# Kernel optimization log

Hardware: AMD Instinct MI355X
Metric: run time of the kernel (lower is better)

The kernel has to match this reference:

```python
import jax, jax.numpy as jnp
import numpy as np

K = 16          # num clusters
DZ = 64         # dim_zt == dim_zi (required by decoder matmul)
DT = 1024       # treatment feature dim (dim_t)
NT = 2048       # number of treatments == dim_x (columns of input_ins)
NI = 4096       # number of instances
MU_P_WT = 5.0
COS_EPS = 1e-6


def setup_inputs() -> dict:
    key = jax.random.key(0)
    ks = jax.random.split(key, 12)
    s = 0.02
    return {
        "input_ins": jax.random.uniform(ks[0], (NI, NT), dtype=jnp.float32),
        "input_treat": jax.random.normal(ks[1], (NT, DT), dtype=jnp.float32),
        # nn.Linear params (torch layout: W [out, in], y = x @ W.T + b)
        "W_mu_zt": jax.random.normal(ks[2], (DZ, DT)) * s,
        "b_mu_zt": jnp.zeros((DZ,), jnp.float32),
        "W_lv_zt": jax.random.normal(ks[3], (DZ, DT)) * s,
        "b_lv_zt": jnp.zeros((DZ,), jnp.float32),
        "W_arec": jax.random.normal(ks[4], (DT, DZ)) * s,
        "b_arec": jnp.zeros((DT,), jnp.float32),
        "W_mu_zi": jax.random.normal(ks[5], (DZ, NT)) * s,
        "b_mu_zi": jnp.zeros((DZ,), jnp.float32),
        "W_lv_zi": jax.random.normal(ks[6], (DZ, NT)) * s,
        "b_lv_zi": jnp.zeros((DZ,), jnp.float32),
        "mu_p_zt": jax.random.normal(ks[7], (K, DZ), dtype=jnp.float32),
        "logvar_p_zt": jnp.ones((K, DZ), jnp.float32),
        "W_y1": jax.random.normal(ks[8], (K * DZ, DZ)) * s,
        "b_y1": jnp.zeros((K * DZ,), jnp.float32),
        "W_y2": jax.random.normal(ks[9], (1, K * DZ)) * s,
        "b_y2": jnp.zeros((1,), jnp.float32),
    }


def reference(input_ins, input_treat, W_mu_zt, b_mu_zt, W_lv_zt, b_lv_zt,
              W_arec, b_arec, W_mu_zi, b_mu_zi, W_lv_zi, b_lv_zi,
              mu_p_zt, logvar_p_zt, W_y1, b_y1, W_y2, b_y2):
    # encode_t (eval mode: zt_sample = mu_zt)
    mu_zt = input_treat @ W_mu_zt.T + b_mu_zt           # [NT, DZ]
    logvar_zt = input_treat @ W_lv_zt.T + b_lv_zt       # [NT, DZ]
    zt = mu_zt

    # compute_qc (cosine similarity vs scaled cluster centers, *10)
    centers = MU_P_WT * mu_p_zt                          # [K, DZ]
    num = zt @ centers.T                                 # [NT, K]
    denom = jnp.maximum(
        jnp.linalg.norm(zt, axis=1, keepdims=True) * jnp.linalg.norm(centers, axis=1)[None, :],
        COS_EPS)
    qc_raw = 10.0 * num / denom                          # [NT, K]
    cates = jax.nn.softmax(qc_raw, axis=1)               # forward softmaxes qc once
    c_sample = jax.nn.softmax(cates, axis=1)             # encode_i (eval) softmaxes again

    # encode_i, vectorized over K clusters: (input_ins * cates_k) @ W.T + b
    # fused einsum avoids materializing the [K, NI, NT] masked inputs
    mu_zi = jnp.einsum('nt,tk,dt->knd', input_ins, c_sample, W_mu_zi) + b_mu_zi       # [K, NI, DZ]
    logvar_zi = jnp.einsum('nt,tk,dt->knd', input_ins, c_sample, W_lv_zi) + b_lv_zi   # [K, NI, DZ]
    zi = mu_zi  # eval-mode reparameterize

    # a_reconstby_zt
    a_reconst = jax.nn.sigmoid(zt @ W_arec.T + b_arec)   # [NT, DT]

    # decoder: sum_k sigmoid(zi_k @ zt.T) * cates_k
    logits = jnp.einsum('knd,td->knt', zi, zt)           # [K, NI, NT]
    a_pred = jnp.einsum('knt,tk->nt', jax.nn.sigmoid(logits), c_sample)  # [NI, NT]

    # predictY
    zi_all = jnp.transpose(zi, (1, 0, 2)).reshape(zi.shape[1], K * DZ)   # cat over k, dim=1
    a_zt = input_ins @ zt                                # [NI, DZ]
    rep_w1 = a_zt @ W_y1.T + b_y1                        # [NI, K*DZ]
    pred_y2 = zi_all @ W_y2.T + b_y2                     # [NI, 1]
    # diag(rep_w1 @ zi_all.T) == rowwise dot product (no NIxNI matmul)
    mu_y = jnp.sum(rep_w1 * zi_all, axis=1, keepdims=True) + pred_y2     # [NI, 1]
    logvar_y = jnp.ones_like(mu_y)

    return (mu_zt, logvar_zt, mu_p_zt, logvar_p_zt, cates, mu_zi, logvar_zi,
            zi, a_pred, mu_y, logvar_y, a_reconst)
```

## Files before the change

### kernel.cpp

```cpp
#include <hip/hip_runtime.h>

typedef unsigned short ushort_t;
typedef unsigned int   uint32;
typedef __attribute__((ext_vector_type(8))) short short8;
typedef __attribute__((ext_vector_type(4))) float f32x4;

#define DEV __device__ __forceinline__

#define KC 16
#define DZ 64
#define DT 1024
#define NT 2048
#define NI 4096
#define KD 1024

#define O_MU_ZT   0
#define O_LV_ZT   131072
#define O_MU_P    262144
#define O_LV_P    263168
#define O_CATES   264192
#define O_MU_ZI   296960
#define O_LV_ZI   4491264
#define O_ZI      8685568
#define O_APRED   12879872
#define O_MU_Y    21268480
#define O_LV_Y    21272576
#define O_AREC    21276672

#define WSF_ZT   0
#define WSF_C    131072
#define WSF_CT   163840
#define WSF_AZT  196608
#define WSF_END  458752
#define WSU_ZTB  0
#define WSU_BC   131072
#define WSU_ZIB  4325376
#define WSU_INSB 8519680
#define WSU_ZHT  16908288
#define WSU_ZLT  17039360

DEV ushort_t f2b(float f){
  uint32 u = __float_as_uint(f);
  u += 0x7fffu + ((u >> 16) & 1u);
  return (ushort_t)(u >> 16);
}
DEV uint32 pk(float lo, float hi){
  return (__float_as_uint(hi) & 0xffff0000u) | (__float_as_uint(lo) >> 16);
}
DEV float wred64(float v){
#pragma unroll
  for (int m = 32; m; m >>= 1) v += __shfl_xor(v, m, 64);
  return v;
}
DEV float fastrcp(float x){ return __builtin_amdgcn_rcpf(x); }
DEV void gl2lds16(ushort_t* l, const ushort_t* g){
  __builtin_amdgcn_global_load_lds(
      (const __attribute__((address_space(1))) unsigned int*)g,
      (__attribute__((address_space(3))) unsigned int*)l, 16, 0, 0);
}

__global__ __launch_bounds__(256) void k_encode_t(
    const float* __restrict__ treat, const float* __restrict__ Wmu,
    const float* __restrict__ bmu, const float* __restrict__ Wlv,
    const float* __restrict__ blv, float* __restrict__ out,
    float* __restrict__ ws_zt)
{
  __shared__ float rowsh[8 * DT];
  const int n0 = blockIdx.x * 8, tid = threadIdx.x;
  const float4* src = (const float4*)(treat + (size_t)n0 * DT);
#pragma unroll
  for (int i = 0; i < 8; ++i)
    ((float4*)rowsh)[tid + i * 256] = src[tid + i * 256];
  __syncthreads();
  const int j = tid & 127, half = tid >> 7;
  const bool isMu = j < 64;
  const int jj = j & 63;
  const float* W = (isMu ? Wmu : Wlv) + (size_t)jj * DT;
  const float bias = isMu ? bmu[jj] : blv[jj];
  float a0 = bias, a1 = bias, a2 = bias, a3 = bias;
  const float4* w4 = (const float4*)W;
  const float4* r0 = (const float4*)&rowsh[(half*4 + 0) * DT];
  const float4* r1 = (const float4*)&rowsh[(half*4 + 1) * DT];
  const float4* r2 = (const float4*)&rowsh[(half*4 + 2) * DT];
  const float4* r3 = (const float4*)&rowsh[(half*4 + 3) * DT];
#pragma unroll 4
  for (int i = 0; i < DT / 4; ++i){
    float4 wv = w4[i];
    float4 v0 = r0[i], v1 = r1[i], v2 = r2[i], v3 = r3[i];
    a0 += wv.x*v0.x + wv.y*v0.y + wv.z*v0.z + wv.w*v0.w;
    a1 += wv.x*v1.x + wv.y*v1.y + wv.z*v1.z + wv.w*v1.w;
    a2 += wv.x*v2.x + wv.y*v2.y + wv.z*v2.z + wv.w*v2.w;
    a3 += wv.x*v3.x + wv.y*v3.y + wv.z*v3.z + wv.w*v3.w;
  }
  float acc[4] = {a0, a1, a2, a3};
#pragma unroll
  for (int r = 0; r < 4; ++r){
    const int row = n0 + half*4 + r;
    if (isMu){ out[O_MU_ZT + row*DZ + jj] = acc[r]; ws_zt[row*DZ + jj] = acc[r]; }
    else     { out[O_LV_ZT + row*DZ + jj] = acc[r]; }
  }
}

__global__ __launch_bounds__(256) void k_qc(
    const float* __restrict__ mu_p, const float* __restrict__ ws_zt,
    float* __restrict__ out, float* __restrict__ ws_c, float* __restrict__ ws_cT)
{
  const int tid = threadIdx.x, lane = tid & 63;
  const int row = blockIdx.x * 4 + (tid >> 6);
  const float z = ws_zt[row * DZ + lane];
  const float nz = sqrtf(wred64(z * z));
  float myqc = 0.f;
#pragma unroll
  for (int k = 0; k < KC; ++k){
    float cv  = 5.f * mu_p[k * DZ + lane];
    float dot = wred64(z * cv);
    float nc2 = wred64(cv * cv);
    float qc  = 10.f * dot / fmaxf(nz * sqrtf(nc2), 1e-6f);
    if (lane == k) myqc = qc;
  }
  float mx = myqc;
#pragma unroll
  for (int m = 8; m; m >>= 1) mx = fmaxf(mx, __shfl_xor(mx, m, 16));
  float e = __expf(myqc - mx);
  float s = e;
#pragma unroll
  for (int m = 8; m; m >>= 1) s += __shfl_xor(s, m, 16);
  float cates = e / s;
  float mx2 = cates;
#pragma unroll
  for (int m = 8; m; m >>= 1) mx2 = fmaxf(mx2, __shfl_xor(mx2, m, 16));
  float e2 = __expf(cates - mx2);
  float s2 = e2;
#pragma unroll
  for (int m = 8; m; m >>= 1) s2 += __shfl_xor(s2, m, 16);
  float c2 = e2 / s2;
  if (lane < KC){
    out[O_CATES + row * KC + lane] = cates;
    ws_c[row * KC + lane] = c2;
    ws_cT[lane * NT + row] = c2;
  }
}

__global__ __launch_bounds__(256) void k_prep(
    const float* __restrict__ Wmu, const float* __restrict__ Wlv,
    const float* __restrict__ cT, const float* __restrict__ zt,
    const float* __restrict__ ins,
    ushort_t* __restrict__ Bc, ushort_t* __restrict__ ztb,
    ushort_t* __restrict__ insb,
    ushort_t* __restrict__ zhT, ushort_t* __restrict__ zlT,
    const float* __restrict__ mu_p, const float* __restrict__ lv_p,
    float* __restrict__ out)
{
  const int bx = blockIdx.x, tid = threadIdx.x;
  if (bx < 2048){
    const int j = bx;
    const bool isMu = j < KD;
    const int kk = (j & (KD-1)) >> 6, d = j & 63;
    const float* W = (isMu ? Wmu : Wlv) + (size_t)d * NT;
    const float* c = cT + (size_t)kk * NT;
    const int t = tid * 8;
    float4 w0 = *(const float4*)(W + t), w1 = *(const float4*)(W + t + 4);
    float4 c0 = *(const float4*)(c + t), c1 = *(const float4*)(c + t + 4);
    ushort_t v[8];
    v[0]=f2b(w0.x*c0.x); v[1]=f2b(w0.y*c0.y); v[2]=f2b(w0.z*c0.z); v[3]=f2b(w0.w*c0.w);
    v[4]=f2b(w1.x*c1.x); v[5]=f2b(w1.y*c1.y); v[6]=f2b(w1.z*c1.z); v[7]=f2b(w1.w*c1.w);
    *(uint4*)(Bc + (size_t)j * NT + t) = *(uint4*)v;
  } else if (bx < 2080){
    const int g = (bx - 2048) * 256 + tid;
    const int base = g * 16;
    const float4* src = (const float4*)(zt + base);
    float4 z0 = src[0], z1 = src[1], z2 = src[2], z3 = src[3];
    ushort_t v[16];
    v[0]=f2b(z0.x); v[1]=f2b(z0.y); v[2]=f2b(z0.z); v[3]=f2b(z0.w);
    v[4]=f2b(z1.x); v[5]=f2b(z1.y); v[6]=f2b(z1.z); v[7]=f2b(z1.w);
    v[8]=f2b(z2.x); v[9]=f2b(z2.y); v[10]=f2b(z2.z); v[11]=f2b(z2.w);
    v[12]=f2b(z3.x); v[13]=f2b(z3.y); v[14]=f2b(z3.z); v[15]=f2b(z3.w);
    *(uint4*)(ztb + base) = *(uint4*)&v[0];
    *(uint4*)(ztb + base + 8) = *(uint4*)&v[8];
  } else if (bx < 2084){
    const int i = (bx - 2080) * 256 + tid;
    out[O_MU_P + i] = mu_p[i];
    out[O_LV_P + i] = lv_p[i];
  } else if (bx < 4132){
    const int g = (bx - 2084) * 256 + tid;
    const int base = g * 16;
    const float4* src = (const float4*)(ins + base);
    float4 z0 = src[0], z1 = src[1], z2 = src[2], z3 = src[3];
    ushort_t v[16];
    v[0]=f2b(z0.x); v[1]=f2b(z0.y); v[2]=f2b(z0.z); v[3]=f2b(z0.w);
    v[4]=f2b(z1.x); v[5]=f2b(z1.y); v[6]=f2b(z1.z); v[7]=f2b(z1.w);
    v[8]=f2b(z2.x); v[9]=f2b(z2.y); v[10]=f2b(z2.z); v[11]=f2b(z2.w);
    v[12]=f2b(z3.x); v[13]=f2b(z3.y); v[14]=f2b(z3.z); v[15]=f2b(z3.w);
    *(uint4*)(insb + base) = *(uint4*)&v[0];
    *(uint4*)(insb + base + 8) = *(uint4*)&v[8];
  } else {
    __shared__ float zsh[64 * 65];
    const int t0 = (bx - 4132) * 64;
#pragma unroll
    for (int jj = 0; jj < 16; ++jj){
      const int idx = jj * 256 + tid;
      const int t = idx >> 6, d = idx & 63;
      zsh[t * 65 + d] = zt[(size_t)(t0 + t) * DZ + d];
    }
    __syncthreads();
    const int d = tid >> 2, tq = tid & 3;
    ushort_t vh[16], vl[16];
#pragma unroll
    for (int i = 0; i < 16; ++i){
      const float f = zsh[(tq * 16 + i) * 65 + d];
      const uint32 u = __float_as_uint(f);
      vh[i] = (ushort_t)(u >> 16);
      const float hf = __uint_as_float(u & 0xffff0000u);
      vl[i] = (ushort_t)(__float_as_uint(f - hf) >> 16);
    }
    *(uint4*)(zhT + (size_t)d * NT + t0 + tq * 16)     = *(uint4*)&vh[0];
    *(uint4*)(zhT + (size_t)d * NT + t0 + tq * 16 + 8) = *(uint4*)&vh[8];
    *(uint4*)(zlT + (size_t)d * NT + t0 + tq * 16)     = *(uint4*)&vl[0];
    *(uint4*)(zlT + (size_t)d * NT + t0 + tq * 16 + 8) = *(uint4*)&vl[8];
  }
}

__global__ __launch_bounds__(256) void k_encode_i(
    const ushort_t* __restrict__ insb, const ushort_t* __restrict__ Bc,
    const float* __restrict__ bmu, const float* __restrict__ blv,
    float* __restrict__ out, ushort_t* __restrict__ zib)
{
  __shared__ ushort_t As[2*128*64];
  __shared__ ushort_t Bs[2*128*64];
  const int tid = threadIdx.x;
  const int orig = blockIdx.y * 16 + blockIdx.x;
  const int swz  = (orig & 7) * 64 + (orig >> 3);
  const int j0 = (swz & 15) * 128, n0 = (swz >> 4) * 128;
  const int w = tid >> 6, lane = tid & 63;
  const int wm = w & 1, wn = w >> 1;
  const int l16 = lane & 15, quad = lane >> 4;

  const int srow = tid >> 3, schunk = (tid & 7) ^ (srow & 7);
  const ushort_t* aSrc = insb + (size_t)(n0 + srow) * NT + schunk * 8;
  const ushort_t* bSrc = Bc  + (size_t)(j0 + srow) * NT + schunk * 8;

  f32x4 acc[4][4] = {};

#pragma unroll
  for (int i = 0; i < 4; ++i){
    gl2lds16(&As[tid*8] + i * 2048, aSrc + (size_t)i * 32 * NT);
    gl2lds16(&Bs[tid*8] + i * 2048, bSrc + (size_t)i * 32 * NT);
  }
  __syncthreads();

  int cur = 0;
  for (int kt = 0; kt < NT/64; ++kt){
    if (kt < NT/64 - 1){
      const ushort_t* ak = aSrc + (kt+1) * 64;
      const ushort_t* bk = bSrc + (kt+1) * 64;
      ushort_t* ad = &As[(cur^1)*8192 + tid*8];
      ushort_t* bd = &Bs[(cur^1)*8192 + tid*8];
#pragma unroll
      for (int i = 0; i < 4; ++i){
        gl2lds16(ad + i * 2048, ak + (size_t)i * 32 * NT);
        gl2lds16(bd + i * 2048, bk + (size_t)i * 32 * NT);
      }
    }
    const ushort_t* Ab = &As[cur*8192];
    const ushort_t* Bb = &Bs[cur*8192];
#pragma unroll
    for (int ks = 0; ks < 2; ++ks){
      const int rsw = ((ks*4 + quad) ^ (l16 & 7)) * 8;
      short8 af[4], bf[4];
#pragma unroll
      for (int mf = 0; mf < 4; ++mf)
        af[mf] = *(const short8*)&Ab[(wm*64 + mf*16 + l16)*64 + rsw];
#pragma unroll
      for (int nf = 0; nf < 4; ++nf)
        bf[nf] = *(const short8*)&Bb[(wn*64 + nf*16 + l16)*64 + rsw];
      __builtin_amdgcn_s_setprio(1);
#pragma unroll
      for (int mf = 0; mf < 4; ++mf)
#pragma unroll
        for (int nf = 0; nf < 4; ++nf)
          acc[mf][nf] = __builtin_amdgcn_mfma_f32_16x16x32_bf16(af[mf], bf[nf], acc[mf][nf], 0, 0, 0);
      __builtin_amdgcn_s_setprio(0);
    }
    __syncthreads();
    cur ^= 1;
  }

  const int colW = j0 + wn * 64;
  const bool isMu = colW < KD;
  const int kk = (colW & (KD - 1)) >> 6;
  const float* bias = isMu ? bmu : blv;
  const size_t zbase = (size_t)kk * (NI * DZ);
#pragma unroll
  for (int mf = 0; mf < 4; ++mf){
    const int r = n0 + wm*64 + mf*16 + quad*4;
#pragma unroll
    for (int nf = 0; nf < 4; ++nf){
      const int d = nf*16 + l16;
      const float bv = bias[d];
#pragma unroll
      for (int reg = 0; reg < 4; ++reg){
        float v = acc[mf][nf][reg] + bv;
        size_t idx = zbase + (size_t)(r + reg)*DZ + d;
        if (isMu){
          out[O_MU_ZI + idx] = v;
          out[O_ZI + idx] = v;
          zib[idx] = f2b(v);
        } else {
          out[O_LV_ZI + idx] = v;
        }
      }
    }
  }
}

__global__ __launch_bounds__(256) void k_decoder(
    const ushort_t* __restrict__ ztb, const ushort_t* __restrict__ zib,
    const float* __restrict__ ws_c, float* __restrict__ out)
{
  __shared__ ushort_t Zt[64*64];
  __shared__ ushort_t Zi[128*64];
  __shared__ float ct[64*17];
  const int tid = threadIdx.x;
  const int t0 = blockIdx.x * 64, n0 = blockIdx.y * 128;
  const int w = tid >> 6, lane = tid & 63;
  const int wm = w & 1, wn = w >> 1;
  const int l16 = lane & 15, quad = lane >> 4;
  const int zr = tid >> 2, zq = tid & 3;
  const int ir = tid >> 1, ih = tid & 1;
  {
    const uint4* src = (const uint4*)(ztb + (size_t)(t0 + zr)*DZ + zq*16);
    uint4 z0 = src[0], z1 = src[1];
    ushort_t* dst = &Zt[zr*64];
    *(uint4*)&dst[((zq*2 + 0) ^ (zr & 7)) * 8] = z0;
    *(uint4*)&dst[((zq*2 + 1) ^ (zr & 7)) * 8] = z1;
  }
  for (int i = tid; i < 64*16; i += 256){
    int t = i >> 4, k = i & 15;
    ct[t*17 + k] = ws_c[(size_t)(t0 + t)*KC + k];
  }
  const ushort_t* iG = zib + (size_t)(n0 + ir)*DZ + ih*32;
  ushort_t* isw = &Zi[ir*64];
  const int sw0 = ((ih*4 + 0) ^ (ir & 7)) * 8;
  const int sw1 = ((ih*4 + 1) ^ (ir & 7)) * 8;
  const int sw2 = ((ih*4 + 2) ^ (ir & 7)) * 8;
  const int sw3 = ((ih*4 + 3) ^ (ir & 7)) * 8;
  uint4 Zr0, Zr1, Zr2, Zr3;
  {
    const uint4* zp = (const uint4*)iG;
    Zr0 = zp[0]; Zr1 = zp[1]; Zr2 = zp[2]; Zr3 = zp[3];
  }
  f32x4 accum[4][2] = {};
  for (int k = 0; k < KC; ++k){
    __syncthreads();
    *(uint4*)&isw[sw0] = Zr0; *(uint4*)&isw[sw1] = Zr1;
    *(uint4*)&isw[sw2] = Zr2; *(uint4*)&isw[sw3] = Zr3;
    __syncthreads();
    if (k < KC - 1){
      const uint4* zp = (const uint4*)(iG + (size_t)(k+1)*(NI*DZ));
      Zr0 = zp[0]; Zr1 = zp[1]; Zr2 = zp[2]; Zr3 = zp[3];
    }
    f32x4 s[4][2] = {};
#pragma unroll
    for (int ks = 0; ks < 2; ++ks){
      const int rsw = ((ks*4 + quad) ^ (l16 & 7)) * 8;
      short8 af[4], bf[2];
#pragma unroll
      for (int mf = 0; mf < 4; ++mf)
        af[mf] = *(const short8*)&Zi[(wm*64 + mf*16 + l16)*64 + rsw];
#pragma unroll
      for (int nf = 0; nf < 2; ++nf)
        bf[nf] = *(const short8*)&Zt[(wn*32 + nf*16 + l16)*64 + rsw];
#pragma unroll
      for (int mf = 0; mf < 4; ++mf)
#pragma unroll
        for (int nf = 0; nf < 2; ++nf)
          s[mf][nf] = __builtin_amdgcn_mfma_f32_16x16x32_bf16(af[mf], bf[nf], s[mf][nf], 0, 0, 0);
    }
#pragma unroll
    for (int nf = 0; nf < 2; ++nf){
      const float cv = ct[(wn*32 + nf*16 + l16)*17 + k];
#pragma unroll
      for (int mf = 0; mf < 4; ++mf)
#pragma unroll
        for (int reg = 0; reg < 4; ++reg)
          accum[mf][nf][reg] += cv * fastrcp(1.f + __expf(-s[mf][nf][reg]));
    }
  }
#pragma unroll
  for (int mf = 0; mf < 4; ++mf){
    const int r = n0 + wm*64 + mf*16 + quad*4;
#pragma unroll
    for (int nf = 0; nf < 2; ++nf){
      const int col = t0 + wn*32 + nf*16 + l16;
#pragma unroll
      for (int reg = 0; reg < 4; ++reg)
        out[O_APRED + (size_t)(r + reg)*NT + col] = accum[mf][nf][reg];
    }
  }
}

__global__ __launch_bounds__(256) void k_arec(
    const float* __restrict__ ws_zt, const float* __restrict__ W,
    const float* __restrict__ bias, float* __restrict__ out)
{
  __shared__ float zsh[8 * DZ];
  const int n0 = blockIdx.x * 8, tid = threadIdx.x;
  if (tid < 128)
    ((float4*)zsh)[tid] = ((const float4*)(ws_zt + (size_t)n0 * DZ))[tid];
  __syncthreads();
#pragma unroll
  for (int jo = 0; jo < 4; ++jo){
    const int j = jo*256 + tid;
    const float4* w4 = (const float4*)(W + (size_t)j * DZ);
    const float b = bias[j];
    float acc[8];
#pragma unroll
    for (int r = 0; r < 8; ++r) acc[r] = b;
#pragma unroll
    for (int i = 0; i < 16; ++i){
      float4 wv = w4[i];
#pragma unroll
      for (int r = 0; r < 8; ++r){
        const float* z = &zsh[r*DZ + i*4];
        acc[r] += wv.x*z[0] + wv.y*z[1] + wv.z*z[2] + wv.w*z[3];
      }
    }
#pragma unroll
    for (int r = 0; r < 8; ++r)
      out[O_AREC + (size_t)(n0 + r)*DT + j] = fastrcp(1.f + __expf(-acc[r]));
  }
}

__global__ __launch_bounds__(256) void k_azt(
    const float* __restrict__ ins, const ushort_t* __restrict__ zhT,
    const ushort_t* __restrict__ zlT, float* __restrict__ azt)
{
  const int tid = threadIdx.x;
  const int n0 = blockIdx.x * 16;
  const int w = tid >> 6, lane = tid & 63;
  const int l16 = lane & 15, quad = lane >> 4;
  const float* aRow = ins + (size_t)(n0 + l16) * NT + quad * 8;
  const ushort_t* bh = zhT + (size_t)(w * 16 + l16) * NT + quad * 8;
  const ushort_t* bl = zlT + (size_t)(w * 16 + l16) * NT + quad * 8;
  f32x4 acc = {};
#pragma unroll 4
  for (int kt = 0; kt < 32; ++kt){
#pragma unroll
    for (int ks = 0; ks < 2; ++ks){
      const int ko = kt * 64 + ks * 32;
      float4 a0 = *(const float4*)(aRow + ko);
      float4 a1 = *(const float4*)(aRow + ko + 4);
      uint32 u0 = __float_as_uint(a0.x), u1 = __float_as_uint(a0.y);
      uint32 u2 = __float_as_uint(a0.z), u3 = __float_as_uint(a0.w);
      uint32 u4 = __float_as_uint(a1.x), u5 = __float_as_uint(a1.y);
      uint32 u6 = __float_as_uint(a1.z), u7 = __float_as_uint(a1.w);
      uint4 H, L;
      H.x = (u1 & 0xffff0000u) | (u0 >> 16);
      H.y = (u3 & 0xffff0000u) | (u2 >> 16);
      H.z = (u5 & 0xffff0000u) | (u4 >> 16);
      H.w = (u7 & 0xffff0000u) | (u6 >> 16);
      float l0 = a0.x - __uint_as_float(u0 & 0xffff0000u);
      float l1 = a0.y - __uint_as_float(u1 & 0xffff0000u);
      float l2 = a0.z - __uint_as_float(u2 & 0xffff0000u);
      float l3 = a0.w - __uint_as_float(u3 & 0xffff0000u);
      float l4 = a1.x - __uint_as_float(u4 & 0xffff0000u);
      float l5 = a1.y - __uint_as_float(u5 & 0xffff0000u);
      float l6 = a1.z - __uint_as_float(u6 & 0xffff0000u);
      float l7 = a1.w - __uint_as_float(u7 & 0xffff0000u);
      L.x = pk(l0, l1); L.y = pk(l2, l3); L.z = pk(l4, l5); L.w = pk(l6, l7);
      short8 ah = *(short8*)&H, al = *(short8*)&L;
      short8 bh8 = *(const short8*)(bh + ko);
      short8 bl8 = *(const short8*)(bl + ko);
      acc = __builtin_amdgcn_mfma_f32_16x16x32_bf16(ah, bh8, acc, 0, 0, 0);
      acc = __builtin_amdgcn_mfma_f32_16x16x32_bf16(al, bh8, acc, 0, 0, 0);
      acc = __builtin_amdgcn_mfma_f32_16x16x32_bf16(ah, bl8, acc, 0, 0, 0);
    }
  }
  const int col = w * 16 + l16;
#pragma unroll
  for (int reg = 0; reg < 4; ++reg)
    azt[(size_t)(n0 + quad * 4 + reg) * DZ + col] = acc[reg];
}

__global__ __launch_bounds__(256) void k_muy(
    const float* __restrict__ azt, const float* __restrict__ Wy1,
    const float* __restrict__ by1, const float* __restrict__ Wy2,
    const float* __restrict__ by2, const float* __restrict__ zi_out,
    float* __restrict__ out)
{
  __shared__ float sazt[16][DZ];
  const int tid = threadIdx.x;
  const int n0 = blockIdx.x * 16;
  for (int i = tid; i < 16*DZ; i += 256)
    sazt[i >> 6][i & 63] = azt[(size_t)(n0 + (i >> 6))*DZ + (i & 63)];
  __syncthreads();
  const int w = tid >> 6, lane = tid & 63;
  float s0 = 0.f, s1 = 0.f, s2 = 0.f, s3 = 0.f;
  for (int jj = 0; jj < 16; ++jj){
    const int j = jj*64 + lane;
    const float4* wr = (const float4*)(Wy1 + (size_t)j * DZ);
    float d0 = 0.f, d1 = 0.f, d2 = 0.f, d3 = 0.f;
    const float* a0 = sazt[w*4 + 0];
    const float* a1 = sazt[w*4 + 1];
    const float* a2 = sazt[w*4 + 2];
    const float* a3 = sazt[w*4 + 3];
#pragma unroll
    for (int i = 0; i < 16; ++i){
      float4 wv = wr[i];
      d0 += wv.x*a0[i*4] + wv.y*a0[i*4+1] + wv.z*a0[i*4+2] + wv.w*a0[i*4+3];
      d1 += wv.x*a1[i*4] + wv.y*a1[i*4+1] + wv.z*a1[i*4+2] + wv.w*a1[i*4+3];
      d2 += wv.x*a2[i*4] + wv.y*a2[i*4+1] + wv.z*a2[i*4+2] + wv.w*a2[i*4+3];
      d3 += wv.x*a3[i*4] + wv.y*a3[i*4+1] + wv.z*a3[i*4+2] + wv.w*a3[i*4+3];
    }
    const float add = by1[j] + Wy2[j];
    const size_t zb = (size_t)jj*(NI*DZ) + lane;
    s0 += (d0 + add) * zi_out[zb + (size_t)(n0 + w*4 + 0)*DZ];
    s1 += (d1 + add) * zi_out[zb + (size_t)(n0 + w*4 + 1)*DZ];
    s2 += (d2 + add) * zi_out[zb + (size_t)(n0 + w*4 + 2)*DZ];
    s3 += (d3 + add) * zi_out[zb + (size_t)(n0 + w*4 + 3)*DZ];
  }
  s0 = wred64(s0); s1 = wred64(s1); s2 = wred64(s2); s3 = wred64(s3);
  if (lane == 0){
    const float b = by2[0];
    out[O_MU_Y + n0 + w*4 + 0] = s0 + b;
    out[O_MU_Y + n0 + w*4 + 1] = s1 + b;
    out[O_MU_Y + n0 + w*4 + 2] = s2 + b;
    out[O_MU_Y + n0 + w*4 + 3] = s3 + b;
  }
  if (tid < 16) out[O_LV_Y + n0 + tid] = 1.0f;
}

extern "C" void kernel_launch(void* const* d_in, const int* in_sizes, int n_in,
                              void* d_out, int out_size, void* d_ws, size_t ws_size,
                              hipStream_t stream)
{
  (void)in_sizes; (void)n_in; (void)out_size; (void)ws_size;
  const float* ins   = (const float*)d_in[0];
  const float* treat = (const float*)d_in[1];
  const float* Wmzt  = (const float*)d_in[2];
  const float* bmzt  = (const float*)d_in[3];
  const float* Wlzt  = (const float*)d_in[4];
  const float* blzt  = (const float*)d_in[5];
  const float* Warec = (const float*)d_in[6];
  const float* barec = (const float*)d_in[7];
  const float* Wmzi  = (const float*)d_in[8];
  const float* bmzi  = (const float*)d_in[9];
  const float* Wlzi  = (const float*)d_in[10];
  const float* blzi  = (const float*)d_in[11];
  const float* mu_p  = (const float*)d_in[12];
  const float* lv_p  = (const float*)d_in[13];
  const float* Wy1   = (const float*)d_in[14];
  const float* by1   = (const float*)d_in[15];
  const float* Wy2   = (const float*)d_in[16];
  const float* by2   = (const float*)d_in[17];
  float* out = (float*)d_out;
  float* wsf = (float*)d_ws;
  ushort_t* wsu = (ushort_t*)(wsf + WSF_END);

  float* ws_zt  = wsf + WSF_ZT;
  float* ws_c   = wsf + WSF_C;
  float* ws_cT  = wsf + WSF_CT;
  float* ws_azt = wsf + WSF_AZT;
  ushort_t* ztb  = wsu + WSU_ZTB;
  ushort_t* Bc   = wsu + WSU_BC;
  ushort_t* zib  = wsu + WSU_ZIB;
  ushort_t* insb = wsu + WSU_INSB;
  ushort_t* zhT  = wsu + WSU_ZHT;
  ushort_t* zlT  = wsu + WSU_ZLT;

  k_encode_t<<<NT/8, 256, 0, stream>>>(treat, Wmzt, bmzt, Wlzt, blzt, out, ws_zt);
  k_qc      <<<NT/4, 256, 0, stream>>>(mu_p, ws_zt, out, ws_c, ws_cT);
  k_prep    <<<4164, 256, 0, stream>>>(Wmzi, Wlzi, ws_cT, ws_zt, ins, Bc, ztb, insb, zhT, zlT, mu_p, lv_p, out);
  k_encode_i<<<dim3(16, 32), 256, 0, stream>>>(insb, Bc, bmzi, blzi, out, zib);
  k_decoder <<<dim3(32, 32), 256, 0, stream>>>(ztb, zib, ws_c, out);
  k_arec    <<<NT/8, 256, 0, stream>>>(ws_zt, Warec, barec, out);
  k_azt     <<<NI/16, 256, 0, stream>>>(ins, zhT, zlT, ws_azt);
  k_muy     <<<NI/16, 256, 0, stream>>>(ws_azt, Wy1, by1, Wy2, by2, out + O_ZI, out);
}
```

Measured before the change: 413.6 us.

## Hoist decoder Zt fragments and widen small kernels to 512 threads

The decoder now loads the loop-invariant Zt B-fragments from shared memory once into registers instead of reloading them for every cluster iteration. k_arec, k_azt and k_muy move to 512-thread blocks. k_azt splits its K dimension across two wave groups and combines the two halves through shared memory. k_muy gives each wave 2 rows instead of 4. The aim is fewer LDS reads in the decoder and more parallelism in the small tail kernels, at the cost of extra registers and one more barrier.

```diff
diff --git a/kernel.cpp b/kernel.cpp
--- a/kernel.cpp
+++ b/kernel.cpp
@@ -338,6 +338,15 @@
     int t = i >> 4, k = i & 15;
     ct[t*17 + k] = ws_c[(size_t)(t0 + t)*KC + k];
   }
+  __syncthreads();
+  short8 bfh[2][2];
+#pragma unroll
+  for (int ks = 0; ks < 2; ++ks){
+    const int rsw = ((ks*4 + quad) ^ (l16 & 7)) * 8;
+#pragma unroll
+    for (int nf = 0; nf < 2; ++nf)
+      bfh[ks][nf] = *(const short8*)&Zt[(wn*32 + nf*16 + l16)*64 + rsw];
+  }
   const ushort_t* iG = zib + (size_t)(n0 + ir)*DZ + ih*32;
   ushort_t* isw = &Zi[ir*64];
   const int sw0 = ((ih*4 + 0) ^ (ir & 7)) * 8;
@@ -363,18 +372,15 @@
 #pragma unroll
     for (int ks = 0; ks < 2; ++ks){
       const int rsw = ((ks*4 + quad) ^ (l16 & 7)) * 8;
-      short8 af[4], bf[2];
+      short8 af[4];
 #pragma unroll
       for (int mf = 0; mf < 4; ++mf)
         af[mf] = *(const short8*)&Zi[(wm*64 + mf*16 + l16)*64 + rsw];
 #pragma unroll
-      for (int nf = 0; nf < 2; ++nf)
-        bf[nf] = *(const short8*)&Zt[(wn*32 + nf*16 + l16)*64 + rsw];
-#pragma unroll
       for (int mf = 0; mf < 4; ++mf)
 #pragma unroll
         for (int nf = 0; nf < 2; ++nf)
-          s[mf][nf] = __builtin_amdgcn_mfma_f32_16x16x32_bf16(af[mf], bf[nf], s[mf][nf], 0, 0, 0);
+          s[mf][nf] = __builtin_amdgcn_mfma_f32_16x16x32_bf16(af[mf], bfh[ks][nf], s[mf][nf], 0, 0, 0);
     }
 #pragma unroll
     for (int nf = 0; nf < 2; ++nf){
@@ -399,7 +405,7 @@
   }
 }
 
-__global__ __launch_bounds__(256) void k_arec(
+__global__ __launch_bounds__(512) void k_arec(
     const float* __restrict__ ws_zt, const float* __restrict__ W,
     const float* __restrict__ bias, float* __restrict__ out)
 {
@@ -409,8 +415,8 @@
     ((float4*)zsh)[tid] = ((const float4*)(ws_zt + (size_t)n0 * DZ))[tid];
   __syncthreads();
 #pragma unroll
-  for (int jo = 0; jo < 4; ++jo){
-    const int j = jo*256 + tid;
+  for (int jo = 0; jo < 2; ++jo){
+    const int j = jo*512 + tid;
     const float4* w4 = (const float4*)(W + (size_t)j * DZ);
     const float b = bias[j];
     float acc[8];
@@ -431,20 +437,22 @@
   }
 }
 
-__global__ __launch_bounds__(256) void k_azt(
+__global__ __launch_bounds__(512) void k_azt(
     const float* __restrict__ ins, const ushort_t* __restrict__ zhT,
     const ushort_t* __restrict__ zlT, float* __restrict__ azt)
 {
+  __shared__ float red[16*64];
   const int tid = threadIdx.x;
   const int n0 = blockIdx.x * 16;
   const int w = tid >> 6, lane = tid & 63;
+  const int kh = w >> 2, wd = w & 3;
   const int l16 = lane & 15, quad = lane >> 4;
-  const float* aRow = ins + (size_t)(n0 + l16) * NT + quad * 8;
-  const ushort_t* bh = zhT + (size_t)(w * 16 + l16) * NT + quad * 8;
-  const ushort_t* bl = zlT + (size_t)(w * 16 + l16) * NT + quad * 8;
+  const float* aRow = ins + (size_t)(n0 + l16) * NT + kh * 1024 + quad * 8;
+  const ushort_t* bh = zhT + (size_t)(wd * 16 + l16) * NT + kh * 1024 + quad * 8;
+  const ushort_t* bl = zlT + (size_t)(wd * 16 + l16) * NT + kh * 1024 + quad * 8;
   f32x4 acc = {};
 #pragma unroll 4
-  for (int kt = 0; kt < 32; ++kt){
+  for (int kt = 0; kt < 16; ++kt){
 #pragma unroll
     for (int ks = 0; ks < 2; ++ks){
       const int ko = kt * 64 + ks * 32;
@@ -476,13 +484,21 @@
       acc = __builtin_amdgcn_mfma_f32_16x16x32_bf16(ah, bl8, acc, 0, 0, 0);
     }
   }
-  const int col = w * 16 + l16;
-#pragma unroll
-  for (int reg = 0; reg < 4; ++reg)
-    azt[(size_t)(n0 + quad * 4 + reg) * DZ + col] = acc[reg];
-}
-
-__global__ __launch_bounds__(256) void k_muy(
+  const int col = wd * 16 + l16;
+  if (kh == 1){
+#pragma unroll
+    for (int reg = 0; reg < 4; ++reg)
+      red[(quad*4 + reg)*64 + col] = acc[reg];
+  }
+  __syncthreads();
+  if (kh == 0){
+#pragma unroll
+    for (int reg = 0; reg < 4; ++reg)
+      azt[(size_t)(n0 + quad*4 + reg) * DZ + col] = acc[reg] + red[(quad*4 + reg)*64 + col];
+  }
+}
+
+__global__ __launch_bounds__(512) void k_muy(
     const float* __restrict__ azt, const float* __restrict__ Wy1,
     const float* __restrict__ by1, const float* __restrict__ Wy2,
     const float* __restrict__ by2, const float* __restrict__ zi_out,
@@ -491,41 +507,33 @@
   __shared__ float sazt[16][DZ];
   const int tid = threadIdx.x;
   const int n0 = blockIdx.x * 16;
-  for (int i = tid; i < 16*DZ; i += 256)
+  for (int i = tid; i < 16*DZ; i += 512)
     sazt[i >> 6][i & 63] = azt[(size_t)(n0 + (i >> 6))*DZ + (i & 63)];
   __syncthreads();
   const int w = tid >> 6, lane = tid & 63;
-  float s0 = 0.f, s1 = 0.f, s2 = 0.f, s3 = 0.f;
+  float s0 = 0.f, s1 = 0.f;
   for (int jj = 0; jj < 16; ++jj){
     const int j = jj*64 + lane;
     const float4* wr = (const float4*)(Wy1 + (size_t)j * DZ);
-    float d0 = 0.f, d1 = 0.f, d2 = 0.f, d3 = 0.f;
-    const float* a0 = sazt[w*4 + 0];
-    const float* a1 = sazt[w*4 + 1];
-    const float* a2 = sazt[w*4 + 2];
-    const float* a3 = sazt[w*4 + 3];
+    float d0 = 0.f, d1 = 0.f;
+    const float* a0 = sazt[w*2 + 0];
+    const float* a1 = sazt[w*2 + 1];
 #pragma unroll
     for (int i = 0; i < 16; ++i){
       float4 wv = wr[i];
       d0 += wv.x*a0[i*4] + wv.y*a0[i*4+1] + wv.z*a0[i*4+2] + wv.w*a0[i*4+3];
       d1 += wv.x*a1[i*4] + wv.y*a1[i*4+1] + wv.z*a1[i*4+2] + wv.w*a1[i*4+3];
-      d2 += wv.x*a2[i*4] + wv.y*a2[i*4+1] + wv.z*a2[i*4+2] + wv.w*a2[i*4+3];
-      d3 += wv.x*a3[i*4] + wv.y*a3[i*4+1] + wv.z*a3[i*4+2] + wv.w*a3[i*4+3];
     }
     const float add = by1[j] + Wy2[j];
     const size_t zb = (size_t)jj*(NI*DZ) + lane;
-    s0 += (d0 + add) * zi_out[zb + (size_t)(n0 + w*4 + 0)*DZ];
-    s1 += (d1 + add) * zi_out[zb + (size_t)(n0 + w*4 + 1)*DZ];
-    s2 += (d2 + add) * zi_out[zb + (size_t)(n0 + w*4 + 2)*DZ];
-    s3 += (d3 + add) * zi_out[zb + (size_t)(n0 + w*4 + 3)*DZ];
-  }
-  s0 = wred64(s0); s1 = wred64(s1); s2 = wred64(s2); s3 = wred64(s3);
+    s0 += (d0 + add) * zi_out[zb + (size_t)(n0 + w*2 + 0)*DZ];
+    s1 += (d1 + add) * zi_out[zb + (size_t)(n0 + w*2 + 1)*DZ];
+  }
+  s0 = wred64(s0); s1 = wred64(s1);
   if (lane == 0){
     const float b = by2[0];
-    out[O_MU_Y + n0 + w*4 + 0] = s0 + b;
-    out[O_MU_Y + n0 + w*4 + 1] = s1 + b;
-    out[O_MU_Y + n0 + w*4 + 2] = s2 + b;
-    out[O_MU_Y + n0 + w*4 + 3] = s3 + b;
+    out[O_MU_Y + n0 + w*2 + 0] = s0 + b;
+    out[O_MU_Y + n0 + w*2 + 1] = s1 + b;
   }
   if (tid < 16) out[O_LV_Y + n0 + tid] = 1.0f;
 }
@@ -573,7 +581,7 @@
   k_prep    <<<4164, 256, 0, stream>>>(Wmzi, Wlzi, ws_cT, ws_zt, ins, Bc, ztb, insb, zhT, zlT, mu_p, lv_p, out);
   k_encode_i<<<dim3(16, 32), 256, 0, stream>>>(insb, Bc, bmzi, blzi, out, zib);
   k_decoder <<<dim3(32, 32), 256, 0, stream>>>(ztb, zib, ws_c, out);
-  k_arec    <<<NT/8, 256, 0, stream>>>(ws_zt, Warec, barec, out);
-  k_azt     <<<NI/16, 256, 0, stream>>>(ins, zhT, zlT, ws_azt);
-  k_muy     <<<NI/16, 256, 0, stream>>>(ws_azt, Wy1, by1, Wy2, by2, out + O_ZI, out);
-}
+  k_arec    <<<NT/8, 512, 0, stream>>>(ws_zt, Warec, barec, out);
+  k_azt     <<<NI/16, 512, 0, stream>>>(ins, zhT, zlT, ws_azt);
+  k_muy     <<<NI/16, 512, 0, stream>>>(ws_azt, Wy1, by1, Wy2, by2, out + O_ZI, out);
+}
```

After: 426.9 us. 3.2% more time.
